# Kernel optimization log

Measured on AMD Instinct MI355X. Metric: run time of the kernel, lower is better.

The kernel has to match this reference:

```python
import jax, jax.numpy as jnp
import numpy as np

NUM_ITERATIONS = 3
EPS = 1e-12  # matches torch F.normalize default eps


def setup_inputs() -> dict:
    key = jax.random.key(0)
    k1, k2 = jax.random.split(key)
    B, IN_CAPS, IN_LEN = 64, 1152, 8
    OUT_CAPS, OUT_LEN = 64, 16
    x = jax.random.normal(k1, (B, IN_CAPS, IN_LEN), dtype=jnp.float32)
    # xavier_uniform over (out_caps, out_len, in_len): fan_in=in_len, fan_out=out_len
    limit = float(np.sqrt(6.0 / (IN_LEN + OUT_LEN)))
    weight = jax.random.uniform(k2, (OUT_CAPS, OUT_LEN, IN_LEN), dtype=jnp.float32,
                                minval=-limit, maxval=limit)
    return {"x": x, "weight": weight}


def reference(x, weight):
    # priors[b,o,n,l] = sum_i weight[o,l,i] * x[b,n,i]  -> [B, out_caps, in_caps, out_len]
    priors = jnp.einsum('oli,bni->bonl', weight, x)
    # k-means routing, similarity='dot', squash=False (module defaults)
    out = jnp.mean(priors, axis=-2, keepdims=True)  # [B, O, 1, L] initial centroid
    probs = None
    for _ in range(NUM_ITERATIONS):
        norm = jnp.linalg.norm(out, axis=-1, keepdims=True)
        out_n = out / jnp.maximum(norm, EPS)  # F.normalize(output, dim=-1)
        logits = jnp.sum(priors * out_n, axis=-1, keepdims=True)  # [B, O, N, 1]
        probs = jax.nn.softmax(logits, axis=-2)  # softmax over in_capsules
        out = jnp.sum(probs * priors, axis=-2, keepdims=True)  # [B, O, 1, L]
    # squash=False -> return raw centroid
    return out.squeeze(-2), probs.squeeze(-1)  # [B, O, L], [B, O, N]
```

## Files before the change

### kernel.cpp

```cpp
#include <hip/hip_runtime.h>
#include <math.h>


#define NCAPS 1152
#define ILEN  8
#define OCAPS 64
#define OLEN  16
#define T     512
#define NWAVE 8
#define TPW   9
#define NITER 3
#define OG    16
#define XT_PITCH 1156
#define E_PITCH  1160

typedef __attribute__((ext_vector_type(8))) short short8;
typedef __attribute__((ext_vector_type(4))) float f32x4;

__device__ __forceinline__ unsigned f2bf_u(float f) {
    unsigned u = __builtin_bit_cast(unsigned, f);
    return (u + 0x7FFFu + ((u >> 16) & 1u)) >> 16;
}
__device__ __forceinline__ unsigned pack2(float a, float b) {
    return f2bf_u(a) | (f2bf_u(b) << 16);
}
__device__ __forceinline__ float bf2f(unsigned h) {
    return __builtin_bit_cast(float, h << 16);
}
__device__ __forceinline__ short8 s8_from(unsigned a, unsigned b, unsigned c, unsigned d) {
    uint4 t = make_uint4(a, b, c, d);
    return __builtin_bit_cast(short8, t);
}

template<int CTRL>
__device__ __forceinline__ float dpp_add(float x) {
    int xi = __builtin_bit_cast(int, x);
    int r  = __builtin_amdgcn_update_dpp(0, xi, CTRL, 0xf, 0xf, true);
    return x + __builtin_bit_cast(float, r);
}
__device__ __forceinline__ float wave_sum63(float v) {
    v = dpp_add<0x111>(v);
    v = dpp_add<0x112>(v);
    v = dpp_add<0x114>(v);
    v = dpp_add<0x118>(v);
    v = dpp_add<0x142>(v);
    v = dpp_add<0x143>(v);
    return v;
}
__device__ __forceinline__ float allsum16(float v) {
    v = dpp_add<0xB1>(v);
    v = dpp_add<0x4E>(v);
    v = dpp_add<0x124>(v);
    v = dpp_add<0x128>(v);
    return v;
}

__global__ __launch_bounds__(T, 2) void caps_kernel(const float* __restrict__ x,
                                                    const float* __restrict__ w,
                                                    float* __restrict__ dout,
                                                    int probs_base) {
    const int tid  = threadIdx.x;
    const int lane = tid & 63;
    const int wid  = tid >> 6;
    const int l16  = lane & 15;
    const int quad = lane >> 4;
    const bool q0  = (quad == 0);
    const int b  = blockIdx.x >> 2;
    const int og = blockIdx.x & 3;

    __shared__ __align__(16) unsigned short pool[NCAPS * ILEN + 10 * XT_PITCH];
    __shared__ __align__(16) unsigned short Yl[OLEN][16];
    __shared__ __align__(16) float Wl[OG][OLEN][ILEN];
    __shared__ __align__(16) float Scmb[NWAVE][OLEN][17];
    __shared__ float ZL[OG];
    unsigned short* xA    = pool;
    unsigned short* xaugT = pool + NCAPS * ILEN;

    ((float4*)&Wl[0][0][0])[tid] = ((const float4*)(w + (size_t)og * OG * OLEN * ILEN))[tid];

    float a0 = 0.f, a1 = 0.f, a2 = 0.f, a3 = 0.f;
    float a4 = 0.f, a5 = 0.f, a6 = 0.f, a7 = 0.f;
    const float4* xs = (const float4*)(x + (size_t)b * NCAPS * ILEN);
    #pragma unroll
    for (int p = 0; p < 3; ++p) {
        const int row = p * T + tid;
        if (row < NCAPS) {
            float4 x0 = xs[row * 2], x1 = xs[row * 2 + 1];
            a0 += x0.x; a1 += x0.y; a2 += x0.z; a3 += x0.w;
            a4 += x1.x; a5 += x1.y; a6 += x1.z; a7 += x1.w;
            unsigned h0 = f2bf_u(x0.x), h1 = f2bf_u(x0.y), h2 = f2bf_u(x0.z), h3 = f2bf_u(x0.w);
            unsigned h4 = f2bf_u(x1.x), h5 = f2bf_u(x1.y), h6 = f2bf_u(x1.z), h7 = f2bf_u(x1.w);
            *(uint4*)&xA[row * ILEN] = make_uint4(h0 | (h1 << 16), h2 | (h3 << 16),
                                                  h4 | (h5 << 16), h6 | (h7 << 16));
            xaugT[0 * XT_PITCH + row] = (unsigned short)h0;
            xaugT[1 * XT_PITCH + row] = (unsigned short)h1;
            xaugT[2 * XT_PITCH + row] = (unsigned short)h2;
            xaugT[3 * XT_PITCH + row] = (unsigned short)h3;
            xaugT[4 * XT_PITCH + row] = (unsigned short)h4;
            xaugT[5 * XT_PITCH + row] = (unsigned short)h5;
            xaugT[6 * XT_PITCH + row] = (unsigned short)h6;
            xaugT[7 * XT_PITCH + row] = (unsigned short)h7;
            xaugT[8 * XT_PITCH + row] = 0x3F80;
        }
    }
    for (int idx = tid; idx < XT_PITCH; idx += T) xaugT[9 * XT_PITCH + idx] = 0;

    a0 = wave_sum63(a0); a1 = wave_sum63(a1); a2 = wave_sum63(a2); a3 = wave_sum63(a3);
    a4 = wave_sum63(a4); a5 = wave_sum63(a5); a6 = wave_sum63(a6); a7 = wave_sum63(a7);
    if (lane == 63) {
        Scmb[wid][0][0] = a0; Scmb[wid][0][1] = a1;
        Scmb[wid][0][2] = a2; Scmb[wid][0][3] = a3;
        Scmb[wid][0][4] = a4; Scmb[wid][0][5] = a5;
        Scmb[wid][0][6] = a6; Scmb[wid][0][7] = a7;
    }
    __syncthreads();

    const int jr = (l16 < 9) ? l16 : 9;
    const unsigned short* xTw = xaugT + jr * XT_PITCH + wid * (TPW * 16) + 4 * quad;
    const unsigned short* xAw = xA + (wid * (TPW * 16) + l16) * ILEN;
    const short8 zs = {0, 0, 0, 0, 0, 0, 0, 0};
    const f32x4  zc = {0.f, 0.f, 0.f, 0.f};

    unsigned st0[TPW], st1[TPW];

    #pragma unroll
    for (int it = 0; it <= NITER; ++it) {
        if (it > 0) {
            short8 bL = q0 ? *(const short8*)&Yl[l16][0] : zs;
            f32x4 sacc = zc;
            #pragma unroll
            for (int tt = 0; tt < TPW; ++tt) {
                uint2 t2 = *(const uint2*)(xTw + tt * 16);
                short8 bs = s8_from(t2.x, t2.y, 0u, 0u);
                short8 aL = q0 ? *(const short8*)(xAw + tt * 128) : zs;
                f32x4 d = __builtin_amdgcn_mfma_f32_16x16x32_bf16(aL, bL, zc, 0, 0, 0);
                float e0 = __expf(d[0]), e1 = __expf(d[1]);
                float e2 = __expf(d[2]), e3 = __expf(d[3]);
                unsigned p0 = pack2(e0, e1), p1 = pack2(e2, e3);
                if (it == NITER) { st0[tt] = p0; st1[tt] = p1; }
                short8 as = s8_from(p0, p1, 0u, 0u);
                sacc = __builtin_amdgcn_mfma_f32_16x16x32_bf16(as, bs, sacc, 0, 0, 0);
            }
            #pragma unroll
            for (int r = 0; r < 4; ++r) Scmb[wid][4 * quad + r][l16] = sacc[r];
            __syncthreads();
        }

        if (tid < 256) {
            const int o = tid >> 4, l = tid & 15;
            float sv[9];
            if (it == 0) {
                #pragma unroll
                for (int i = 0; i < 8; ++i) {
                    float t = Scmb[0][0][i];
                    #pragma unroll
                    for (int ww = 1; ww < NWAVE; ++ww) t += Scmb[ww][0][i];
                    sv[i] = t;
                }
                sv[8] = (float)NCAPS;
            } else {
                #pragma unroll
                for (int i = 0; i < 9; ++i) {
                    float t = Scmb[0][o][i];
                    #pragma unroll
                    for (int ww = 1; ww < NWAVE; ++ww) t += Scmb[ww][o][i];
                    sv[i] = t;
                }
            }
            const float zinv = 1.0f / sv[8];
            const float* wrow = &Wl[o][l][0];
            float outl = wrow[0] * sv[0];
            #pragma unroll
            for (int i = 1; i < ILEN; ++i) outl = fmaf(wrow[i], sv[i], outl);
            outl *= zinv;

            if (it < NITER) {
                float n2 = allsum16(outl * outl);
                const float inv = 1.0f / fmaxf(sqrtf(n2), 1e-12f);
                const float oh = outl * inv;
                #pragma unroll
                for (int i = 0; i < ILEN; ++i) {
                    float yi = allsum16(wrow[i] * oh);
                    if (l == i) Yl[o][i] = (unsigned short)f2bf_u(yi);
                }
            } else {
                dout[(((size_t)(b * OCAPS + og * OG + o)) << 4) + l] = outl;
                if (l == 0) ZL[o] = zinv;
            }
        }

        if (it == NITER) {
            unsigned short* eL = pool;
            const int n0 = wid * (TPW * 16) + 4 * quad;
            #pragma unroll
            for (int tt = 0; tt < TPW; ++tt) {
                *(unsigned*)&eL[l16 * E_PITCH + n0 + tt * 16]     = st0[tt];
                *(unsigned*)&eL[l16 * E_PITCH + n0 + tt * 16 + 2] = st1[tt];
            }
        }
        __syncthreads();
    }

    {
        const unsigned short* eL = pool;
        const int o  = tid >> 5;
        const int c0 = tid & 31;
        const float zi = ZL[o];
        float* pp = dout + (size_t)probs_base + (size_t)(b * OCAPS + og * OG + o) * NCAPS;
        #pragma unroll
        for (int j = 0; j < 9; ++j) {
            const int c = c0 + 32 * j;
            uint2 t = *(const uint2*)&eL[o * E_PITCH + 4 * c];
            float4 v;
            v.x = bf2f(t.x & 0xFFFFu) * zi;
            v.y = bf2f(t.x >> 16) * zi;
            v.z = bf2f(t.y & 0xFFFFu) * zi;
            v.w = bf2f(t.y >> 16) * zi;
            ((float4*)pp)[c] = v;
        }
    }
}

extern "C" void kernel_launch(void* const* d_in, const int* in_sizes, int n_in,
                              void* d_out, int out_size, void* d_ws, size_t ws_size,
                              hipStream_t stream) {
    const float* x = (const float*)d_in[0];
    const float* w = (const float*)d_in[1];
    float* out = (float*)d_out;
    const int Bv = in_sizes[0] / (NCAPS * ILEN);
    const int nblocks = Bv * (OCAPS / OG);
    const int probs_base = Bv * OCAPS * OLEN;
    caps_kernel<<<dim3(nblocks), dim3(T), 0, stream>>>(x, w, out, probs_base);
}
```

Measured before the change: 72.33 us.

## Use 12 waves per block with 6 tiles each and transposed reduction buffer

Raises the block size from 512 to 768 threads (12 waves, 6 capsule tiles per wave) so the routing loop is split across more waves, and raises the launch bound to 3 blocks per CU. The per-wave partial sums buffer is transposed so the cross-wave reduction reads contiguous float4 vectors. The x load now handles two rows per thread with packed 32-bit transposed stores, and the probs write-out is remapped over the larger thread count. More waves shorten each wave's serial chain but add register pressure under the tighter launch bound and more threads idle in the 256-thread reduction phase.

```diff
diff --git a/kernel.cpp b/kernel.cpp
--- a/kernel.cpp
+++ b/kernel.cpp
@@ -6,13 +6,14 @@
 #define ILEN  8
 #define OCAPS 64
 #define OLEN  16
-#define T     512
-#define NWAVE 8
-#define TPW   9
+#define T     768
+#define NWAVE 12
+#define TPW   6
 #define NITER 3
 #define OG    16
 #define XT_PITCH 1156
 #define E_PITCH  1160
+#define SC_PITCH 20
 
 typedef __attribute__((ext_vector_type(8))) short short8;
 typedef __attribute__((ext_vector_type(4))) float f32x4;
@@ -55,7 +56,7 @@
     return v;
 }
 
-__global__ __launch_bounds__(T, 2) void caps_kernel(const float* __restrict__ x,
+__global__ __launch_bounds__(T, 3) void caps_kernel(const float* __restrict__ x,
                                                     const float* __restrict__ w,
                                                     float* __restrict__ dout,
                                                     int probs_base) {
@@ -71,47 +72,51 @@
     __shared__ __align__(16) unsigned short pool[NCAPS * ILEN + 10 * XT_PITCH];
     __shared__ __align__(16) unsigned short Yl[OLEN][16];
     __shared__ __align__(16) float Wl[OG][OLEN][ILEN];
-    __shared__ __align__(16) float Scmb[NWAVE][OLEN][17];
+    __shared__ __align__(16) float Scmb[OLEN][OLEN][SC_PITCH];
     __shared__ float ZL[OG];
     unsigned short* xA    = pool;
     unsigned short* xaugT = pool + NCAPS * ILEN;
 
-    ((float4*)&Wl[0][0][0])[tid] = ((const float4*)(w + (size_t)og * OG * OLEN * ILEN))[tid];
+    if (tid < 512)
+        ((float4*)&Wl[0][0][0])[tid] = ((const float4*)(w + (size_t)og * OG * OLEN * ILEN))[tid];
+    if (tid < 128) ((unsigned*)&Yl[0][0])[tid] = 0;
 
     float a0 = 0.f, a1 = 0.f, a2 = 0.f, a3 = 0.f;
     float a4 = 0.f, a5 = 0.f, a6 = 0.f, a7 = 0.f;
-    const float4* xs = (const float4*)(x + (size_t)b * NCAPS * ILEN);
-    #pragma unroll
-    for (int p = 0; p < 3; ++p) {
-        const int row = p * T + tid;
-        if (row < NCAPS) {
-            float4 x0 = xs[row * 2], x1 = xs[row * 2 + 1];
-            a0 += x0.x; a1 += x0.y; a2 += x0.z; a3 += x0.w;
-            a4 += x1.x; a5 += x1.y; a6 += x1.z; a7 += x1.w;
-            unsigned h0 = f2bf_u(x0.x), h1 = f2bf_u(x0.y), h2 = f2bf_u(x0.z), h3 = f2bf_u(x0.w);
-            unsigned h4 = f2bf_u(x1.x), h5 = f2bf_u(x1.y), h6 = f2bf_u(x1.z), h7 = f2bf_u(x1.w);
-            *(uint4*)&xA[row * ILEN] = make_uint4(h0 | (h1 << 16), h2 | (h3 << 16),
-                                                  h4 | (h5 << 16), h6 | (h7 << 16));
-            xaugT[0 * XT_PITCH + row] = (unsigned short)h0;
-            xaugT[1 * XT_PITCH + row] = (unsigned short)h1;
-            xaugT[2 * XT_PITCH + row] = (unsigned short)h2;
-            xaugT[3 * XT_PITCH + row] = (unsigned short)h3;
-            xaugT[4 * XT_PITCH + row] = (unsigned short)h4;
-            xaugT[5 * XT_PITCH + row] = (unsigned short)h5;
-            xaugT[6 * XT_PITCH + row] = (unsigned short)h6;
-            xaugT[7 * XT_PITCH + row] = (unsigned short)h7;
-            xaugT[8 * XT_PITCH + row] = 0x3F80;
-        }
+    if (tid < NCAPS / 2) {
+        const float4* xs = (const float4*)(x + (size_t)b * NCAPS * ILEN);
+        float4 x0 = xs[4 * tid], x1 = xs[4 * tid + 1];
+        float4 x2 = xs[4 * tid + 2], x3 = xs[4 * tid + 3];
+        a0 = x0.x + x2.x; a1 = x0.y + x2.y; a2 = x0.z + x2.z; a3 = x0.w + x2.w;
+        a4 = x1.x + x3.x; a5 = x1.y + x3.y; a6 = x1.z + x3.z; a7 = x1.w + x3.w;
+        unsigned g0 = f2bf_u(x0.x), g1 = f2bf_u(x0.y), g2 = f2bf_u(x0.z), g3 = f2bf_u(x0.w);
+        unsigned g4 = f2bf_u(x1.x), g5 = f2bf_u(x1.y), g6 = f2bf_u(x1.z), g7 = f2bf_u(x1.w);
+        unsigned h0 = f2bf_u(x2.x), h1 = f2bf_u(x2.y), h2 = f2bf_u(x2.z), h3 = f2bf_u(x2.w);
+        unsigned h4 = f2bf_u(x3.x), h5 = f2bf_u(x3.y), h6 = f2bf_u(x3.z), h7 = f2bf_u(x3.w);
+        const int r0 = 2 * tid;
+        *(uint4*)&xA[r0 * ILEN]       = make_uint4(g0 | (g1 << 16), g2 | (g3 << 16),
+                                                   g4 | (g5 << 16), g6 | (g7 << 16));
+        *(uint4*)&xA[(r0 + 1) * ILEN] = make_uint4(h0 | (h1 << 16), h2 | (h3 << 16),
+                                                   h4 | (h5 << 16), h6 | (h7 << 16));
+        *(unsigned*)&xaugT[0 * XT_PITCH + r0] = g0 | (h0 << 16);
+        *(unsigned*)&xaugT[1 * XT_PITCH + r0] = g1 | (h1 << 16);
+        *(unsigned*)&xaugT[2 * XT_PITCH + r0] = g2 | (h2 << 16);
+        *(unsigned*)&xaugT[3 * XT_PITCH + r0] = g3 | (h3 << 16);
+        *(unsigned*)&xaugT[4 * XT_PITCH + r0] = g4 | (h4 << 16);
+        *(unsigned*)&xaugT[5 * XT_PITCH + r0] = g5 | (h5 << 16);
+        *(unsigned*)&xaugT[6 * XT_PITCH + r0] = g6 | (h6 << 16);
+        *(unsigned*)&xaugT[7 * XT_PITCH + r0] = g7 | (h7 << 16);
+        *(unsigned*)&xaugT[8 * XT_PITCH + r0] = 0x3F803F80u;
     }
     for (int idx = tid; idx < XT_PITCH; idx += T) xaugT[9 * XT_PITCH + idx] = 0;
 
     a0 = wave_sum63(a0); a1 = wave_sum63(a1); a2 = wave_sum63(a2); a3 = wave_sum63(a3);
     a4 = wave_sum63(a4); a5 = wave_sum63(a5); a6 = wave_sum63(a6); a7 = wave_sum63(a7);
     if (lane == 63) {
-        Scmb[wid][0][0] = a0; Scmb[wid][0][1] = a1;
-        Scmb[wid][0][2] = a2; Scmb[wid][0][3] = a3;
-        Scmb[wid][0][4] = a4; Scmb[wid][0][5] = a5;
-        Scmb[wid][0][6] = a6; Scmb[wid][0][7] = a7;
+        Scmb[0][0][wid] = a0; Scmb[0][1][wid] = a1;
+        Scmb[0][2][wid] = a2; Scmb[0][3][wid] = a3;
+        Scmb[0][4][wid] = a4; Scmb[0][5][wid] = a5;
+        Scmb[0][6][wid] = a6; Scmb[0][7][wid] = a7;
     }
     __syncthreads();
 
@@ -142,31 +147,24 @@
                 sacc = __builtin_amdgcn_mfma_f32_16x16x32_bf16(as, bs, sacc, 0, 0, 0);
             }
             #pragma unroll
-            for (int r = 0; r < 4; ++r) Scmb[wid][4 * quad + r][l16] = sacc[r];
+            for (int r = 0; r < 4; ++r) Scmb[4 * quad + r][l16][wid] = sacc[r];
             __syncthreads();
         }
 
         if (tid < 256) {
             const int o = tid >> 4, l = tid & 15;
+            const int oi = (it == 0) ? 0 : o;
             float sv[9];
-            if (it == 0) {
-                #pragma unroll
-                for (int i = 0; i < 8; ++i) {
-                    float t = Scmb[0][0][i];
-                    #pragma unroll
-                    for (int ww = 1; ww < NWAVE; ++ww) t += Scmb[ww][0][i];
-                    sv[i] = t;
-                }
-                sv[8] = (float)NCAPS;
-            } else {
-                #pragma unroll
-                for (int i = 0; i < 9; ++i) {
-                    float t = Scmb[0][o][i];
-                    #pragma unroll
-                    for (int ww = 1; ww < NWAVE; ++ww) t += Scmb[ww][o][i];
-                    sv[i] = t;
-                }
-            }
+            #pragma unroll
+            for (int i = 0; i < 9; ++i) {
+                float4 v0 = *(const float4*)&Scmb[oi][i][0];
+                float4 v1 = *(const float4*)&Scmb[oi][i][4];
+                float4 v2 = *(const float4*)&Scmb[oi][i][8];
+                sv[i] = ((v0.x + v0.y) + (v0.z + v0.w))
+                      + ((v1.x + v1.y) + (v1.z + v1.w))
+                      + ((v2.x + v2.y) + (v2.z + v2.w));
+            }
+            if (it == 0) sv[8] = (float)NCAPS;
             const float zinv = 1.0f / sv[8];
             const float* wrow = &Wl[o][l][0];
             float outl = wrow[0] * sv[0];
@@ -203,20 +201,20 @@
 
     {
         const unsigned short* eL = pool;
-        const int o  = tid >> 5;
-        const int c0 = tid & 31;
-        const float zi = ZL[o];
-        float* pp = dout + (size_t)probs_base + (size_t)(b * OCAPS + og * OG + o) * NCAPS;
+        float* pbase = dout + (size_t)probs_base + (size_t)(b * OCAPS + og * OG) * NCAPS;
         #pragma unroll
-        for (int j = 0; j < 9; ++j) {
-            const int c = c0 + 32 * j;
+        for (int j = 0; j < 6; ++j) {
+            const int f = tid + j * T;
+            const int o = f / (NCAPS / 4);
+            const int c = f - o * (NCAPS / 4);
+            const float zi = ZL[o];
             uint2 t = *(const uint2*)&eL[o * E_PITCH + 4 * c];
             float4 v;
             v.x = bf2f(t.x & 0xFFFFu) * zi;
             v.y = bf2f(t.x >> 16) * zi;
             v.z = bf2f(t.y & 0xFFFFu) * zi;
             v.w = bf2f(t.y >> 16) * zi;
-            ((float4*)pp)[c] = v;
+            ((float4*)(pbase + (size_t)o * NCAPS))[c] = v;
         }
     }
 }
```

After: 71.85 us (median of 2 runs). About the same (-0.7%).
